# Performance work log

Measured on AMD Instinct MI355X. Metric: run time of the kernel, lower is better.

Reference implementation:

```python
import jax, jax.numpy as jnp
from jax import lax
import numpy as np

B, T, H, I, O = 256, 2048, 150, 1, 1

def setup_inputs() -> dict:
    key = jax.random.key(0)
    ks = jax.random.split(key, 7)
    s = 1.0 / np.sqrt(H)
    return {
        "input": jax.random.normal(ks[0], (B, T), dtype=jnp.float32),
        "W_ih": jax.random.uniform(ks[1], (3 * H, I), jnp.float32, -s, s),
        "W_hh": jax.random.uniform(ks[2], (3 * H, H), jnp.float32, -s, s),
        "b_ih": jax.random.uniform(ks[3], (3 * H,), jnp.float32, -s, s),
        "b_hh": jax.random.uniform(ks[4], (3 * H,), jnp.float32, -s, s),
        "W_lin": jax.random.uniform(ks[5], (O, H), jnp.float32, -s, s),
        "b_lin": jax.random.uniform(ks[6], (O,), jnp.float32, -s, s),
    }

def reference(input, W_ih, W_hh, b_ih, b_hh, W_lin, b_lin):
    # input: [B, T]; GRUCell recurrence with relu on hidden, per-step linear head.
    hidden = W_hh.shape[1]

    def step(h, x_t):  # h: [B, H], x_t: [B, 1]
        gi = x_t @ W_ih.T + b_ih          # [B, 3H]
        gh = h @ W_hh.T + b_hh            # [B, 3H]
        i_r, i_z, i_n = jnp.split(gi, 3, axis=-1)
        h_r, h_z, h_n = jnp.split(gh, 3, axis=-1)
        r = jax.nn.sigmoid(i_r + h_r)
        z = jax.nn.sigmoid(i_z + h_z)
        n = jnp.tanh(i_n + r * h_n)
        h_new = jax.nn.relu((1.0 - z) * n + z * h)  # relu applied as in original
        y = h_new @ W_lin.T + b_lin       # [B, 1]
        return h_new, y

    xs = jnp.transpose(input)[:, :, None]            # [T, B, 1]
    h0 = jnp.zeros((input.shape[0], hidden), input.dtype)
    _, ys = lax.scan(step, h0, xs)                   # ys: [T, B, 1]
    return jnp.transpose(ys[:, :, 0])                # [B, T] (stack dim=1, squeeze(2))
```

## Files before the change

kernel.cpp:

```cpp
#include <hip/hip_runtime.h>
#include <math.h>


#define BB 256
#define TT 2048
#define HH 150
#define H3 450

typedef float fx2 __attribute__((ext_vector_type(2)));

#define WCLOB \
  "v100","v101","v102","v103","v104","v105","v106","v107","v108","v109", \
  "v110","v111","v112","v113","v114","v115","v116","v117","v118","v119", \
  "v120","v121","v122","v123","v124","v125","v126","v127","v128","v129", \
  "v130","v131","v132","v133","v134","v135","v136","v137","v138","v139", \
  "v140","v141","v142","v143","v144","v145","v146","v147","v148","v149", \
  "v150","v151","v152","v153","v154","v155","v156","v157","v158","v159", \
  "v160","v161","v162","v163","v164","v165","v166","v167","v168","v169", \
  "v170","v171","v172","v173","v174","v175","v176","v177","v178","v179", \
  "v180","v181","v182","v183","v184","v185","v186","v187","v188","v189", \
  "v190","v191","v192","v193","v194","v195","v196","v197","v198","v199", \
  "v200","v201","v202","v203","v204","v205","v206","v207","v208","v209", \
  "v210","v211","v212","v213","v214","v215","v216","v217","v218","v219", \
  "v220","v221","v222","v223","v224","v225","v226","v227","v228","v229", \
  "v230","v231","v232","v233","v234","v235","v236","v237","v238","v239", \
  "v240","v241","v242","v243","v244","v245","v246","v247","v248","v249", \
  "v250","v251"

#define LD4(vA0,vA1,vB0,vB1,OFF) \
  "global_load_dword v" #vA0 ", %[b0], off offset:" #OFF "\n\t" \
  "global_load_dword v" #vA1 ", %[b1], off offset:" #OFF "\n\t" \
  "global_load_dword v" #vB0 ", %[b2], off offset:" #OFF "\n\t" \
  "global_load_dword v" #vB1 ", %[b3], off offset:" #OFF "\n\t"

#define PKB(sp, vp, acc) \
  "v_pk_fma_f32 " acc ", " sp ", " vp ", " acc " op_sel:[0,0,0] op_sel_hi:[0,1,1]\n\t"

#define G4(m0,m1,m2,m3, A0,B0, A1,B1, A2,B2, A3,B3) \
  "v_readlane_b32 s20, %[hq], " #m0 "\n\t" \
  "v_readlane_b32 s22, %[hq], " #m1 "\n\t" \
  "v_readlane_b32 s24, %[hq], " #m2 "\n\t" \
  "v_readlane_b32 s26, %[hq], " #m3 "\n\t" \
  PKB("s[20:21]", A0, "%[a01]") PKB("s[20:21]", B0, "%[a23]") \
  PKB("s[22:23]", A1, "%[a01]") PKB("s[22:23]", B1, "%[a23]") \
  PKB("s[24:25]", A2, "%[a01]") PKB("s[24:25]", B2, "%[a23]") \
  PKB("s[26:27]", A3, "%[a01]") PKB("s[26:27]", B3, "%[a23]")

__global__ __launch_bounds__(512, 2) void gru_seq_kernel(
    const float* __restrict__ input,
    const float* __restrict__ W_ih,
    const float* __restrict__ W_hh,
    const float* __restrict__ b_ih,
    const float* __restrict__ b_hh,
    const float* __restrict__ W_lin,
    const float* __restrict__ b_lin,
    float* __restrict__ out)
{
    const int b    = blockIdx.x;
    const int tid  = threadIdx.x;
    const int lane = tid & 63;
    const int wid  = tid >> 6;
    const int q    = wid & 3;
    const int idx  = ((wid >> 2) << 6) + lane;

    __shared__ float  xrow[TT];
    __shared__ float4 h4[64];
    __shared__ float  PPf[2048];
    __shared__ float  yout[TT];

    ((float4*)xrow)[tid] = ((const float4*)(input + (size_t)b * TT))[tid];
    if (tid < 64) h4[tid] = make_float4(0.f, 0.f, 0.f, 0.f);

    const int r0 = 4 * idx;
#define ROWP(r) ((r) == H3 ? W_lin : W_hh + ((r) < H3 ? (r) : (H3 - 1)) * HH)
    const float* b0 = ROWP(r0)     + q;
    const float* b1 = ROWP(r0 + 1) + q;
    const float* b2 = ROWP(r0 + 2) + q;
    const float* b3 = ROWP(r0 + 3) + q;

    asm volatile(
        LD4(100,101,176,177,0)    LD4(102,103,178,179,16)
        LD4(104,105,180,181,32)   LD4(106,107,182,183,48)
        LD4(108,109,184,185,64)   LD4(110,111,186,187,80)
        LD4(112,113,188,189,96)   LD4(114,115,190,191,112)
        LD4(116,117,192,193,128)  LD4(118,119,194,195,144)
        LD4(120,121,196,197,160)  LD4(122,123,198,199,176)
        LD4(124,125,200,201,192)  LD4(126,127,202,203,208)
        LD4(128,129,204,205,224)  LD4(130,131,206,207,240)
        LD4(132,133,208,209,256)  LD4(134,135,210,211,272)
        LD4(136,137,212,213,288)  LD4(138,139,214,215,304)
        LD4(140,141,216,217,320)  LD4(142,143,218,219,336)
        LD4(144,145,220,221,352)  LD4(146,147,222,223,368)
        LD4(148,149,224,225,384)  LD4(150,151,226,227,400)
        LD4(152,153,228,229,416)  LD4(154,155,230,231,432)
        LD4(156,157,232,233,448)  LD4(158,159,234,235,464)
        LD4(160,161,236,237,480)  LD4(162,163,238,239,496)
        LD4(164,165,240,241,512)  LD4(166,167,242,243,528)
        LD4(168,169,244,245,544)  LD4(170,171,246,247,560)
        LD4(172,173,248,249,576)
        "s_waitcnt vmcnt(0)\n\t"
        :
        : [b0] "v"(b0), [b1] "v"(b1), [b2] "v"(b2), [b3] "v"(b3)
        : WCLOB, "memory");
    {
        const int t37 = (q < 2) ? 148 : 144;
        float w0 = b0[t37], w1 = b1[t37], w2 = b2[t37], w3 = b3[t37];
        asm volatile(
            "v_mov_b32 v174, %0\n\tv_mov_b32 v175, %1\n\t"
            "v_mov_b32 v250, %2\n\tv_mov_b32 v251, %3\n\t"
            :: "v"(w0), "v"(w1), "v"(w2), "v"(w3)
            : "v174","v175","v250","v251");
    }

    float wih_r = 0.f, wih_z = 0.f, wih_n = 0.f;
    float bih_r = 0.f, bih_z = 0.f, bih_n = 0.f;
    float bhh_r = 0.f, bhh_z = 0.f, bhh_n = 0.f;
    if (tid < HH) {
        wih_r = W_ih[tid];          bih_r = b_ih[tid];          bhh_r = b_hh[tid];
        wih_z = W_ih[HH + tid];     bih_z = b_ih[HH + tid];     bhh_z = b_hh[HH + tid];
        wih_n = W_ih[2 * HH + tid]; bih_n = b_ih[2 * HH + tid]; bhh_n = b_hh[2 * HH + tid];
    }
    const float blin = b_lin[0];
    float hreg = 0.f;
    float* outb = out + (size_t)b * TT;
    float2* st01 = (float2*)PPf          + (q << 7) + idx;
    float2* st23 = (float2*)(PPf + 1024) + (q << 7) + idx;
    int ir = 0, iz = 0, in_ = 0;
    if (tid < HH) {
        int r;
        r = tid;        ir  = (((r & 3) >> 1) << 10) + ((r >> 2) << 1) + (r & 1);
        r = HH + tid;   iz  = (((r & 3) >> 1) << 10) + ((r >> 2) << 1) + (r & 1);
        r = 2*HH + tid; in_ = (((r & 3) >> 1) << 10) + ((r >> 2) << 1) + (r & 1);
    }
    const int iy = 1024 + (112 << 1);

    __syncthreads();

    for (int t = 0; t <= TT; ++t) {
        float4 hv = h4[lane];
        float hq = (q == 0) ? hv.x : (q == 1) ? hv.y : (q == 2) ? hv.z : hv.w;
        fx2 a01; a01.x = 0.f; a01.y = 0.f;
        fx2 a23; a23.x = 0.f; a23.y = 0.f;
        asm volatile(
            G4( 0, 1, 2, 3, "v[100:101]","v[176:177]", "v[102:103]","v[178:179]",
                            "v[104:105]","v[180:181]", "v[106:107]","v[182:183]")
            G4( 4, 5, 6, 7, "v[108:109]","v[184:185]", "v[110:111]","v[186:187]",
                            "v[112:113]","v[188:189]", "v[114:115]","v[190:191]")
            G4( 8, 9,10,11, "v[116:117]","v[192:193]", "v[118:119]","v[194:195]",
                            "v[120:121]","v[196:197]", "v[122:123]","v[198:199]")
            G4(12,13,14,15, "v[124:125]","v[200:201]", "v[126:127]","v[202:203]",
                            "v[128:129]","v[204:205]", "v[130:131]","v[206:207]")
            G4(16,17,18,19, "v[132:133]","v[208:209]", "v[134:135]","v[210:211]",
                            "v[136:137]","v[212:213]", "v[138:139]","v[214:215]")
            G4(20,21,22,23, "v[140:141]","v[216:217]", "v[142:143]","v[218:219]",
                            "v[144:145]","v[220:221]", "v[146:147]","v[222:223]")
            G4(24,25,26,27, "v[148:149]","v[224:225]", "v[150:151]","v[226:227]",
                            "v[152:153]","v[228:229]", "v[154:155]","v[230:231]")
            G4(28,29,30,31, "v[156:157]","v[232:233]", "v[158:159]","v[234:235]",
                            "v[160:161]","v[236:237]", "v[162:163]","v[238:239]")
            "v_readlane_b32 s20, %[hq], 32\n\t"
            "v_readlane_b32 s22, %[hq], 33\n\t"
            "v_readlane_b32 s24, %[hq], 34\n\t"
            "v_readlane_b32 s26, %[hq], 35\n\t"
            "v_readlane_b32 s28, %[hq], 36\n\t"
            "v_readlane_b32 s30, %[hq], 37\n\t"
            PKB("s[20:21]", "v[164:165]", "%[a01]")
            PKB("s[20:21]", "v[240:241]", "%[a23]")
            PKB("s[22:23]", "v[166:167]", "%[a01]")
            PKB("s[22:23]", "v[242:243]", "%[a23]")
            PKB("s[24:25]", "v[168:169]", "%[a01]")
            PKB("s[24:25]", "v[244:245]", "%[a23]")
            PKB("s[26:27]", "v[170:171]", "%[a01]")
            PKB("s[26:27]", "v[246:247]", "%[a23]")
            PKB("s[28:29]", "v[172:173]", "%[a01]")
            PKB("s[28:29]", "v[248:249]", "%[a23]")
            PKB("s[30:31]", "v[174:175]", "%[a01]")
            PKB("s[30:31]", "v[250:251]", "%[a23]")
            : [a01] "+v"(a01), [a23] "+v"(a23)
            : [hq] "v"(hq)
            : "s20","s22","s24","s26","s28","s30", WCLOB);
        float2 s0; s0.x = a01.x; s0.y = a01.y;
        float2 s1; s1.x = a23.x; s1.y = a23.y;
        *st01 = s0;
        *st23 = s1;
        __syncthreads();

        if (t < TT && tid < HH) {
            float x  = xrow[t];
            float pr = ((PPf[ir]        + PPf[ir + 256])
                      + (PPf[ir + 512]  + PPf[ir + 768]))  + bhh_r;
            float pz = ((PPf[iz]        + PPf[iz + 256])
                      + (PPf[iz + 512]  + PPf[iz + 768]))  + bhh_z;
            float pn = ((PPf[in_]       + PPf[in_ + 256])
                      + (PPf[in_ + 512] + PPf[in_ + 768])) + bhh_n;
            float gr = fmaf(x, wih_r, bih_r) + pr;
            float gz = fmaf(x, wih_z, bih_z) + pz;
            float r  = 1.f / (1.f + __expf(-gr));
            float z  = 1.f / (1.f + __expf(-gz));
            float ta = fmaf(x, wih_n, bih_n) + r * pn;
            ta = fminf(fmaxf(ta, -15.f), 15.f);
            float e  = __expf(2.f * ta);
            float n  = (e - 1.f) / (e + 1.f);
            float hnew = fmaf(z, hreg - n, n);
            hnew = fmaxf(hnew, 0.f);
            hreg = hnew;
            ((float*)h4)[tid] = hnew;
        }
        if (t > 0 && tid == H3) {
            yout[t - 1] = ((PPf[iy]       + PPf[iy + 256])
                         + (PPf[iy + 512] + PPf[iy + 768])) + blin;
        }
        __syncthreads();
    }

    ((float4*)outb)[tid] = ((const float4*)yout)[tid];
}

extern "C" void kernel_launch(void* const* d_in, const int* in_sizes, int n_in,
                              void* d_out, int out_size, void* d_ws, size_t ws_size,
                              hipStream_t stream) {
    const float* input = (const float*)d_in[0];
    const float* W_ih  = (const float*)d_in[1];
    const float* W_hh  = (const float*)d_in[2];
    const float* b_ih  = (const float*)d_in[3];
    const float* b_hh  = (const float*)d_in[4];
    const float* W_lin = (const float*)d_in[5];
    const float* b_lin = (const float*)d_in[6];
    float* out = (float*)d_out;

    gru_seq_kernel<<<dim3(BB), dim3(512), 0, stream>>>(
        input, W_ih, W_hh, b_ih, b_hh, W_lin, b_lin, out);
}
```

Baseline: 1.832 ms.

## Compute gate update redundantly per wave and double-buffer partials to drop a barrier

Each wave now computes the GRU gate update for the hidden units it owns (j = 4*lane+q) directly in registers, instead of a single group of 150 threads writing h to shared memory for everyone to read back. Partial sums go into a double-buffered shared array, which removes the second __syncthreads per timestep and the h broadcast through LDS. The cost is redundant transcendental gate math across waves and more complex index mapping.

```diff
diff --git a/kernel.cpp b/kernel.cpp
--- a/kernel.cpp
+++ b/kernel.cpp
@@ -63,13 +63,11 @@
     const int q    = wid & 3;
     const int idx  = ((wid >> 2) << 6) + lane;
 
-    __shared__ float  xrow[TT];
-    __shared__ float4 h4[64];
-    __shared__ float  PPf[2048];
-    __shared__ float  yout[TT];
+    __shared__ float xrow[TT];
+    __shared__ float Tbuf[2][2048];
+    __shared__ float yout[TT];
 
     ((float4*)xrow)[tid] = ((const float4*)(input + (size_t)b * TT))[tid];
-    if (tid < 64) h4[tid] = make_float4(0.f, 0.f, 0.f, 0.f);
 
     const int r0 = 4 * idx;
 #define ROWP(r) ((r) == H3 ? W_lin : W_hh + ((r) < H3 ? (r) : (H3 - 1)) * HH)
@@ -112,33 +110,33 @@
             : "v174","v175","v250","v251");
     }
 
-    float wih_r = 0.f, wih_z = 0.f, wih_n = 0.f;
-    float bih_r = 0.f, bih_z = 0.f, bih_n = 0.f;
-    float bhh_r = 0.f, bhh_z = 0.f, bhh_n = 0.f;
-    if (tid < HH) {
-        wih_r = W_ih[tid];          bih_r = b_ih[tid];          bhh_r = b_hh[tid];
-        wih_z = W_ih[HH + tid];     bih_z = b_ih[HH + tid];     bhh_z = b_hh[HH + tid];
-        wih_n = W_ih[2 * HH + tid]; bih_n = b_ih[2 * HH + tid]; bhh_n = b_hh[2 * HH + tid];
-    }
-    const float blin = b_lin[0];
-    float hreg = 0.f;
+    const int m   = (lane < 38) ? lane : 37;
+    const int j   = 4 * lane + q;
+    const int act = (j < HH);
+    const int jc  = act ? j : (HH - 1);
+    const float wih_r = W_ih[jc];          const float bih_r = b_ih[jc];
+    const float bhh_r = b_hh[jc];
+    const float wih_z = W_ih[HH + jc];     const float bih_z = b_ih[HH + jc];
+    const float bhh_z = b_hh[HH + jc];
+    const float wih_n = W_ih[2*HH + jc];   const float bih_n = b_ih[2*HH + jc];
+    const float bhh_n = b_hh[2*HH + jc];
+    const float blin  = b_lin[0];
+
+    const int o_r = q * 128 + m;
+    const int iz  = (q < 2) ? (q + 2) : (q - 2);
+    const int gz  = (q < 2) ? (m + 37) : (m + 38);
+    const int o_z = iz * 128 + gz;
+    const int o_n = q * 128 + m + 75;
+    const int o_y = 2 * 128 + 112;
+
+    float hq = 0.f;
     float* outb = out + (size_t)b * TT;
-    float2* st01 = (float2*)PPf          + (q << 7) + idx;
-    float2* st23 = (float2*)(PPf + 1024) + (q << 7) + idx;
-    int ir = 0, iz = 0, in_ = 0;
-    if (tid < HH) {
-        int r;
-        r = tid;        ir  = (((r & 3) >> 1) << 10) + ((r >> 2) << 1) + (r & 1);
-        r = HH + tid;   iz  = (((r & 3) >> 1) << 10) + ((r >> 2) << 1) + (r & 1);
-        r = 2*HH + tid; in_ = (((r & 3) >> 1) << 10) + ((r >> 2) << 1) + (r & 1);
-    }
-    const int iy = 1024 + (112 << 1);
 
     __syncthreads();
 
     for (int t = 0; t <= TT; ++t) {
-        float4 hv = h4[lane];
-        float hq = (q == 0) ? hv.x : (q == 1) ? hv.y : (q == 2) ? hv.z : hv.w;
+        float* Tc = Tbuf[t & 1];
+
         fx2 a01; a01.x = 0.f; a01.y = 0.f;
         fx2 a23; a23.x = 0.f; a23.y = 0.f;
         asm volatile(
@@ -179,40 +177,42 @@
             : [a01] "+v"(a01), [a23] "+v"(a23)
             : [hq] "v"(hq)
             : "s20","s22","s24","s26","s28","s30", WCLOB);
-        float2 s0; s0.x = a01.x; s0.y = a01.y;
-        float2 s1; s1.x = a23.x; s1.y = a23.y;
-        *st01 = s0;
-        *st23 = s1;
+
+        float* Tw = Tc + (q << 9) + idx;
+        Tw[0]   = a01.x;
+        Tw[128] = a01.y;
+        Tw[256] = a23.x;
+        Tw[384] = a23.y;
         __syncthreads();
 
-        if (t < TT && tid < HH) {
-            float x  = xrow[t];
-            float pr = ((PPf[ir]        + PPf[ir + 256])
-                      + (PPf[ir + 512]  + PPf[ir + 768]))  + bhh_r;
-            float pz = ((PPf[iz]        + PPf[iz + 256])
-                      + (PPf[iz + 512]  + PPf[iz + 768]))  + bhh_z;
-            float pn = ((PPf[in_]       + PPf[in_ + 256])
-                      + (PPf[in_ + 512] + PPf[in_ + 768])) + bhh_n;
+        {
+            int tx = (t < TT) ? t : (TT - 1);
+            float x  = xrow[tx];
+            float pr = ((Tc[o_r]        + Tc[o_r + 512])
+                      + (Tc[o_r + 1024] + Tc[o_r + 1536])) + bhh_r;
+            float pz = ((Tc[o_z]        + Tc[o_z + 512])
+                      + (Tc[o_z + 1024] + Tc[o_z + 1536])) + bhh_z;
+            float pn = ((Tc[o_n]        + Tc[o_n + 1536 - 1024])
+                      + (Tc[o_n + 1024] + Tc[o_n + 1536])) + bhh_n;
             float gr = fmaf(x, wih_r, bih_r) + pr;
-            float gz = fmaf(x, wih_z, bih_z) + pz;
+            float gz_ = fmaf(x, wih_z, bih_z) + pz;
             float r  = 1.f / (1.f + __expf(-gr));
-            float z  = 1.f / (1.f + __expf(-gz));
+            float z  = 1.f / (1.f + __expf(-gz_));
             float ta = fmaf(x, wih_n, bih_n) + r * pn;
             ta = fminf(fmaxf(ta, -15.f), 15.f);
             float e  = __expf(2.f * ta);
             float n  = (e - 1.f) / (e + 1.f);
-            float hnew = fmaf(z, hreg - n, n);
+            float hnew = fmaf(z, hq - n, n);
             hnew = fmaxf(hnew, 0.f);
-            hreg = hnew;
-            ((float*)h4)[tid] = hnew;
+            hq = act ? hnew : 0.f;
         }
-        if (t > 0 && tid == H3) {
-            yout[t - 1] = ((PPf[iy]       + PPf[iy + 256])
-                         + (PPf[iy + 512] + PPf[iy + 768])) + blin;
+        if (tid == 38 && t > 0) {
+            yout[t - 1] = ((Tc[o_y]        + Tc[o_y + 512])
+                         + (Tc[o_y + 1024] + Tc[o_y + 1536])) + blin;
         }
-        __syncthreads();
     }
 
+    __syncthreads();
     ((float4*)outb)[tid] = ((const float4*)yout)[tid];
 }
 
```

Measured after the change: 1.855 ms. Within noise of the previous version (+1.2%).
